# Kernel tuning notes

Hardware: AMD Instinct MI355X
Metric: run time of the kernel (lower is better)

The kernel has to match this reference:

```python
import jax, jax.numpy as jnp
import numpy as np

NUM_EXPERTS = 8
IN_FEATURES = 2048
OUT_FEATURES = 5632
GROUP_SIZE = 64
NUM_TOKENS = 4096


def setup_inputs() -> dict:
    key = jax.random.key(0)
    k1, k2, k3, k4 = jax.random.split(key, 4)
    inp = jax.random.normal(k1, (NUM_TOKENS, IN_FEATURES), dtype=jnp.float32)
    # tokens are pre-sorted contiguously per expert; balanced routing
    tokens_per_expert = jnp.full((NUM_EXPERTS,), NUM_TOKENS // NUM_EXPERTS, dtype=jnp.int32)
    # int4 quantized weights stored as integer codes in [0, 16)
    weights = jax.random.randint(k2, (NUM_EXPERTS, IN_FEATURES, OUT_FEATURES), 0, 16, dtype=jnp.int32)
    n_groups = IN_FEATURES // GROUP_SIZE
    scales = jax.random.uniform(k3, (NUM_EXPERTS, n_groups, OUT_FEATURES, 1), dtype=jnp.float32,
                                minval=0.005, maxval=0.02)
    zeros = jax.random.normal(k4, (NUM_EXPERTS, n_groups, OUT_FEATURES, 1), dtype=jnp.float32) * 0.01
    scales_and_zeros = jnp.concatenate([scales, zeros], axis=-1)  # [E, K//G, N, 2]
    return {"input": inp, "tokens_per_expert": tokens_per_expert,
            "weights": weights, "scales_and_zeros": scales_and_zeros}


def _dequant(weights, scales_and_zeros):
    # torchao int4 convention: w = (q - 8) * scale + zero, grouped along K
    E, K, N = weights.shape
    n_groups = scales_and_zeros.shape[1]
    g = K // n_groups
    q = weights.astype(jnp.float32).reshape(E, n_groups, g, N)
    s = scales_and_zeros[..., 0][:, :, None, :]  # [E, K//G, 1, N]
    z = scales_and_zeros[..., 1][:, :, None, :]
    return ((q - 8.0) * s + z).reshape(E, K, N)


def reference(input, tokens_per_expert, weights, scales_and_zeros):
    num_tokens, K = input.shape
    E = weights.shape[0]
    W = _dequant(weights, scales_and_zeros)  # [E, K, N] float32
    # expert id of each (contiguous-sorted) token from cumsum boundaries
    cum = jnp.cumsum(tokens_per_expert)                      # [E]
    seg = jnp.searchsorted(cum, jnp.arange(num_tokens), side='right')  # [T]
    start = jnp.concatenate([jnp.zeros((1,), cum.dtype), cum[:-1]])
    pos = jnp.arange(num_tokens) - start[seg]                # slot within expert block
    # capacity-based grouped GEMM (balanced routing in setup: C = T // E)
    C = num_tokens // E
    buf = jnp.zeros((E, C, K), input.dtype).at[seg, pos].set(input)
    y = jnp.einsum('eck,ekn->ecn', buf, W)                   # per-expert GEMM
    return y[seg, pos]                                       # [T, N]
```

## Files before the change

kernel.cpp:

```cpp
#include <hip/hip_runtime.h>

#define NE    8
#define KDIM  2048
#define NDIM  5632
#define NTOK  4096
#define CAP   512
#define NGRP  32
#define BM    128
#define BN    128
#define BK    32
#define MT    4
#define NT    44
#define LDSS  40

#define K8      (KDIM / 8)
#define NBLK_N  (NDIM / 256)
#define PACK_BLOCKS (NE * K8 * NBLK_N)
#define ACV_BLOCKS  (NTOK * KDIM / (8 * 256))
#define PACKED_BYTES ((size_t)NE * K8 * NDIM * 4)
#define ABF_BYTES    ((size_t)NTOK * KDIM * 2)

typedef __attribute__((ext_vector_type(8))) short bf16x8;
typedef __attribute__((ext_vector_type(4))) short bf16x4;
typedef __attribute__((ext_vector_type(4))) float f32x4;

static __device__ __forceinline__ short f2bf(float f) {
    union { float f; unsigned u; } x; x.f = f;
    unsigned r = (x.u + 0x7fffu + ((x.u >> 16) & 1u)) >> 16;
    return (short)r;
}

__global__ __launch_bounds__(256)
void pack_kernel(const int* __restrict__ wq, const float* __restrict__ inp,
                 unsigned* __restrict__ pw, unsigned short* __restrict__ abf)
{
    const int bid = blockIdx.x;
    if (bid < PACK_BLOCKS) {
        const int e  = bid / (K8 * NBLK_N);
        const int r  = bid % (K8 * NBLK_N);
        const int k8 = r / NBLK_N;
        const int nb = r % NBLK_N;
        const int n  = nb * 256 + threadIdx.x;
        const int* src = wq + ((size_t)e * KDIM + k8 * 8) * NDIM + n;
        unsigned v = 0;
        #pragma unroll
        for (int j = 0; j < 8; ++j)
            v |= (unsigned)(src[(size_t)j * NDIM] & 15) << (4 * j);
        pw[((size_t)e * K8 + k8) * NDIM + n] = v;
    } else {
        const size_t t = (size_t)(bid - PACK_BLOCKS) * 256 + threadIdx.x;
        const float4* p = (const float4*)inp + t * 2;
        const float4 v0 = p[0], v1 = p[1];
        bf16x8 h;
        h[0] = f2bf(v0.x); h[1] = f2bf(v0.y); h[2] = f2bf(v0.z); h[3] = f2bf(v0.w);
        h[4] = f2bf(v1.x); h[5] = f2bf(v1.y); h[6] = f2bf(v1.z); h[7] = f2bf(v1.w);
        *((bf16x8*)abf + t) = h;
    }
}

__global__ __launch_bounds__(256, 2)
void hqq_gemm2(const unsigned short* __restrict__ abf,
               const unsigned*       __restrict__ pw,
               const float*          __restrict__ sz,
               float*                __restrict__ out)
{
    const int bid = blockIdx.x;
    const int e   = bid / (MT * NT);
    const int rem = bid % (MT * NT);
    const int nt  = rem >> 2;
    const int mt  = rem & 3;

    __shared__ __align__(16) short Alds[BM * LDSS];
    __shared__ __align__(16) short Blds[BN * LDSS];

    const int tid = threadIdx.x;
    const int m0  = e * CAP + mt * BM;
    const int n0  = nt * BN;

    const int a_kq  = tid & 3;
    const int a_row = tid >> 2;
    const int b_n   = tid & 127;
    const int b_h   = tid >> 7;

    const unsigned short* Ab = abf + (size_t)m0 * KDIM;
    const unsigned*       Wb = pw  + (size_t)e * K8 * NDIM + n0 + b_n;
    const float*          SZb = sz + (size_t)e * NGRP * (NDIM * 2) + (size_t)(n0 + b_n) * 2;

    f32x4 acc[4][4];
    #pragma unroll
    for (int i = 0; i < 4; ++i)
        #pragma unroll
        for (int j = 0; j < 4; ++j)
            acc[i][j] = (f32x4){0.f, 0.f, 0.f, 0.f};

    const int wave = tid >> 6;
    const int lane = tid & 63;
    const int wm = (wave >> 1) << 6;
    const int wn = (wave & 1) << 6;
    const int lr = lane & 15;
    const int lq = lane >> 4;

    for (int k0 = 0; k0 < KDIM; k0 += BK) {
        const int g = k0 >> 6;

        #pragma unroll
        for (int p = 0; p < 2; ++p) {
            const int row = a_row + p * 64;
            const bf16x8 v = *(const bf16x8*)(Ab + (size_t)row * KDIM + k0 + a_kq * 8);
            *(bf16x8*)&Alds[row * LDSS + a_kq * 8] = v;
        }

        const float2 s2 = *(const float2*)(SZb + (size_t)g * (NDIM * 2));
        const float s  = s2.x;
        const float z8 = s2.y - 8.f * s2.x;
        const unsigned* wp = Wb + ((size_t)(k0 >> 3) + b_h * 2) * NDIM;
        const unsigned u0 = wp[0];
        const unsigned u1 = wp[NDIM];
        bf16x8 bb0, bb1;
        #pragma unroll
        for (int j = 0; j < 8; ++j) {
            bb0[j] = f2bf(fmaf((float)((u0 >> (4 * j)) & 15u), s, z8));
            bb1[j] = f2bf(fmaf((float)((u1 >> (4 * j)) & 15u), s, z8));
        }
        *(bf16x8*)&Blds[b_n * LDSS + b_h * 16]     = bb0;
        *(bf16x8*)&Blds[b_n * LDSS + b_h * 16 + 8] = bb1;

        __syncthreads();

        bf16x8 af[4], bfv[4];
        #pragma unroll
        for (int i = 0; i < 4; ++i)
            af[i] = *(const bf16x8*)&Alds[(wm + i * 16 + lr) * LDSS + lq * 8];
        #pragma unroll
        for (int j = 0; j < 4; ++j)
            bfv[j] = *(const bf16x8*)&Blds[(wn + j * 16 + lr) * LDSS + lq * 8];
        #pragma unroll
        for (int i = 0; i < 4; ++i)
            #pragma unroll
            for (int j = 0; j < 4; ++j)
                acc[i][j] = __builtin_amdgcn_mfma_f32_16x16x32_bf16(af[i], bfv[j], acc[i][j], 0, 0, 0);

        __syncthreads();
    }

    const int orow0 = m0 + wm + lq * 4;
    const int ocol0 = n0 + wn + lr;
    #pragma unroll
    for (int i = 0; i < 4; ++i)
        #pragma unroll
        for (int r = 0; r < 4; ++r) {
            float* op = out + (size_t)(orow0 + i * 16 + r) * NDIM + ocol0;
            #pragma unroll
            for (int j = 0; j < 4; ++j)
                op[j * 16] = acc[i][j][r];
        }
}

__global__ __launch_bounds__(256, 2)
void hqq_gemm_fallback(const float* __restrict__ inp,
                       const int*   __restrict__ wq,
                       const float* __restrict__ sz,
                       float*       __restrict__ out)
{
    const int bid = blockIdx.x;
    const int e   = bid / (MT * NT);
    const int rem = bid % (MT * NT);
    const int nt  = rem >> 2;
    const int mt  = rem & 3;

    __shared__ __align__(16) short Alds[BM * LDSS];
    __shared__ __align__(16) short Blds[BN * LDSS];

    const int tid = threadIdx.x;
    const int m0  = e * CAP + mt * BM;
    const int n0  = nt * BN;

    const int a_kq  = tid & 7;
    const int a_row = tid >> 3;
    const int b_n   = tid & 127;
    const int b_h   = tid >> 7;

    const float* Ab  = inp + (size_t)m0 * KDIM;
    const int*   Wb  = wq  + (size_t)e * KDIM * NDIM + n0 + b_n;
    const float* SZb = sz  + (size_t)e * NGRP * (NDIM * 2) + (size_t)(n0 + b_n) * 2;

    f32x4 acc[4][4];
    #pragma unroll
    for (int i = 0; i < 4; ++i)
        #pragma unroll
        for (int j = 0; j < 4; ++j)
            acc[i][j] = (f32x4){0.f, 0.f, 0.f, 0.f};

    const int wave = tid >> 6;
    const int lane = tid & 63;
    const int wm = (wave >> 1) << 6;
    const int wn = (wave & 1) << 6;
    const int lr = lane & 15;
    const int lq = lane >> 4;

    for (int k0 = 0; k0 < KDIM; k0 += BK) {
        const int g = k0 >> 6;
        #pragma unroll
        for (int p = 0; p < 4; ++p) {
            const int row = a_row + p * 32;
            const float4 v = *(const float4*)(Ab + (size_t)row * KDIM + k0 + a_kq * 4);
            bf16x4 h;
            h[0] = f2bf(v.x); h[1] = f2bf(v.y); h[2] = f2bf(v.z); h[3] = f2bf(v.w);
            *(bf16x4*)&Alds[row * LDSS + a_kq * 4] = h;
        }
        const float2 s2 = *(const float2*)(SZb + (size_t)g * (NDIM * 2));
        const float s  = s2.x;
        const float z8 = s2.y - 8.f * s2.x;
        #pragma unroll
        for (int oo = 0; oo < 2; ++oo) {
            const int ko = b_h * 8 + oo * 16;
            const int* wp = Wb + (size_t)(k0 + ko) * NDIM;
            bf16x8 bb;
            #pragma unroll
            for (int j = 0; j < 8; ++j) {
                const float q = (float)wp[(size_t)j * NDIM];
                bb[j] = f2bf(fmaf(q, s, z8));
            }
            *(bf16x8*)&Blds[b_n * LDSS + ko] = bb;
        }
        __syncthreads();
        bf16x8 af[4], bfv[4];
        #pragma unroll
        for (int i = 0; i < 4; ++i)
            af[i] = *(const bf16x8*)&Alds[(wm + i * 16 + lr) * LDSS + lq * 8];
        #pragma unroll
        for (int j = 0; j < 4; ++j)
            bfv[j] = *(const bf16x8*)&Blds[(wn + j * 16 + lr) * LDSS + lq * 8];
        #pragma unroll
        for (int i = 0; i < 4; ++i)
            #pragma unroll
            for (int j = 0; j < 4; ++j)
                acc[i][j] = __builtin_amdgcn_mfma_f32_16x16x32_bf16(af[i], bfv[j], acc[i][j], 0, 0, 0);
        __syncthreads();
    }

    const int orow0 = m0 + wm + lq * 4;
    const int ocol0 = n0 + wn + lr;
    #pragma unroll
    for (int i = 0; i < 4; ++i)
        #pragma unroll
        for (int r = 0; r < 4; ++r) {
            float* op = out + (size_t)(orow0 + i * 16 + r) * NDIM + ocol0;
            #pragma unroll
            for (int j = 0; j < 4; ++j)
                op[j * 16] = acc[i][j][r];
        }
}

extern "C" void kernel_launch(void* const* d_in, const int* in_sizes, int n_in,
                              void* d_out, int out_size, void* d_ws, size_t ws_size,
                              hipStream_t stream) {
    const float* inp = (const float*)d_in[0];
    const int*   wq  = (const int*)d_in[2];
    const float* sz  = (const float*)d_in[3];
    float*       out = (float*)d_out;

    if (ws_size >= PACKED_BYTES + ABF_BYTES) {
        unsigned*       pw  = (unsigned*)d_ws;
        unsigned short* abf = (unsigned short*)((char*)d_ws + PACKED_BYTES);
        pack_kernel<<<dim3(PACK_BLOCKS + ACV_BLOCKS), dim3(256), 0, stream>>>(wq, inp, pw, abf);
        hqq_gemm2<<<dim3(NE * MT * NT), dim3(256), 0, stream>>>(abf, pw, sz, out);
    } else {
        hqq_gemm_fallback<<<dim3(NE * MT * NT), dim3(256), 0, stream>>>(inp, wq, sz, out);
    }
}
```

Before: 673.1 us.

## Pre-dequantize weights to transposed bf16 and use direct-to-LDS GEMM loads

```diff
diff --git a/kernel.cpp b/kernel.cpp
--- a/kernel.cpp
+++ b/kernel.cpp
@@ -19,6 +19,11 @@
 #define ACV_BLOCKS  (NTOK * KDIM / (8 * 256))
 #define PACKED_BYTES ((size_t)NE * K8 * NDIM * 4)
 #define ABF_BYTES    ((size_t)NTOK * KDIM * 2)
+#define WBT_BYTES    ((size_t)NE * NDIM * KDIM * 2)
+
+#define KB_DQ (KDIM / 64)
+#define NB_DQ (NDIM / 256)
+#define DQT_BLOCKS (NE * KB_DQ * NB_DQ)
 
 typedef __attribute__((ext_vector_type(8))) short bf16x8;
 typedef __attribute__((ext_vector_type(4))) short bf16x4;
@@ -28,6 +33,127 @@
     union { float f; unsigned u; } x; x.f = f;
     unsigned r = (x.u + 0x7fffu + ((x.u >> 16) & 1u)) >> 16;
     return (short)r;
+}
+
+static __device__ __forceinline__ void gl2lds16(const unsigned short* g, short* l) {
+    __builtin_amdgcn_global_load_lds(
+        (const __attribute__((address_space(1))) unsigned int*)g,
+        (__attribute__((address_space(3))) unsigned int*)l, 16, 0, 0);
+}
+
+__global__ __launch_bounds__(256)
+void dq_kernel(const int* __restrict__ wq, const float* __restrict__ sz,
+               const float* __restrict__ inp,
+               unsigned short* __restrict__ wbt, unsigned short* __restrict__ abf)
+{
+    const int bid = blockIdx.x;
+    if (bid < DQT_BLOCKS) {
+        const int e  = bid / (KB_DQ * NB_DQ);
+        const int r  = bid % (KB_DQ * NB_DQ);
+        const int kb = r / NB_DQ;
+        const int nb = r % NB_DQ;
+        const int n  = nb * 256 + threadIdx.x;
+
+        const int* src = wq + ((size_t)e * KDIM + kb * 64) * NDIM + n;
+        const float2 s2 = *(const float2*)(sz + (((size_t)e * NGRP + kb) * NDIM + n) * 2);
+        const float s  = s2.x;
+        const float z8 = s2.y - 8.f * s2.x;
+        unsigned short* dst = wbt + ((size_t)e * NDIM + n) * KDIM + kb * 64;
+
+        #pragma unroll
+        for (int o = 0; o < 8; ++o) {
+            bf16x8 h;
+            #pragma unroll
+            for (int j = 0; j < 8; ++j) {
+                const float q = (float)src[(size_t)(o * 8 + j) * NDIM];
+                h[j] = f2bf(fmaf(q, s, z8));
+            }
+            *(bf16x8*)(dst + o * 8) = h;
+        }
+    } else {
+        const size_t t = (size_t)(bid - DQT_BLOCKS) * 256 + threadIdx.x;
+        const float4* p = (const float4*)inp + t * 2;
+        const float4 v0 = p[0], v1 = p[1];
+        bf16x8 h;
+        h[0] = f2bf(v0.x); h[1] = f2bf(v0.y); h[2] = f2bf(v0.z); h[3] = f2bf(v0.w);
+        h[4] = f2bf(v1.x); h[5] = f2bf(v1.y); h[6] = f2bf(v1.z); h[7] = f2bf(v1.w);
+        *((bf16x8*)abf + t) = h;
+    }
+}
+
+__global__ __launch_bounds__(256)
+void hqq_gemm3(const unsigned short* __restrict__ abf,
+               const unsigned short* __restrict__ wbt,
+               float* __restrict__ out)
+{
+    const int bid = blockIdx.x;
+    const int e   = bid & 7;
+    const int rem = bid >> 3;
+    const int nt  = rem >> 2;
+    const int mt  = rem & 3;
+
+    __shared__ __align__(16) short Alds[BM * BK];
+    __shared__ __align__(16) short Blds[BN * BK];
+
+    const int tid = threadIdx.x;
+    const int m0  = e * CAP + mt * BM;
+    const int n0  = nt * BN;
+
+    const unsigned short* Ab = abf + (size_t)m0 * KDIM;
+    const unsigned short* Bb = wbt + ((size_t)e * NDIM + n0) * KDIM;
+
+    f32x4 acc[4][4];
+    #pragma unroll
+    for (int i = 0; i < 4; ++i)
+        #pragma unroll
+        for (int j = 0; j < 4; ++j)
+            acc[i][j] = (f32x4){0.f, 0.f, 0.f, 0.f};
+
+    const int wave = tid >> 6;
+    const int lane = tid & 63;
+    const int wm = (wave >> 1) << 6;
+    const int wn = (wave & 1) << 6;
+    const int lr = lane & 15;
+    const int lq = lane >> 4;
+
+    for (int k0 = 0; k0 < KDIM; k0 += BK) {
+        #pragma unroll
+        for (int p = 0; p < 2; ++p) {
+            const int idx = p * 256 + tid;
+            const int row = idx >> 2;
+            const int kq  = idx & 3;
+            gl2lds16(Ab + (size_t)row * KDIM + k0 + kq * 8, &Alds[idx * 8]);
+            gl2lds16(Bb + (size_t)row * KDIM + k0 + kq * 8, &Blds[idx * 8]);
+        }
+        __syncthreads();
+
+        bf16x8 af[4], bv[4];
+        #pragma unroll
+        for (int i = 0; i < 4; ++i)
+            af[i] = *(const bf16x8*)&Alds[(wm + i * 16 + lr) * BK + lq * 8];
+        #pragma unroll
+        for (int j = 0; j < 4; ++j)
+            bv[j] = *(const bf16x8*)&Blds[(wn + j * 16 + lr) * BK + lq * 8];
+        #pragma unroll
+        for (int i = 0; i < 4; ++i)
+            #pragma unroll
+            for (int j = 0; j < 4; ++j)
+                acc[i][j] = __builtin_amdgcn_mfma_f32_16x16x32_bf16(af[i], bv[j], acc[i][j], 0, 0, 0);
+
+        __syncthreads();
+    }
+
+    const int orow0 = m0 + wm + lq * 4;
+    const int ocol0 = n0 + wn + lr;
+    #pragma unroll
+    for (int i = 0; i < 4; ++i)
+        #pragma unroll
+        for (int r = 0; r < 4; ++r) {
+            float* op = out + (size_t)(orow0 + i * 16 + r) * NDIM + ocol0;
+            #pragma unroll
+            for (int j = 0; j < 4; ++j)
+                op[j * 16] = acc[i][j][r];
+        }
 }
 
 __global__ __launch_bounds__(256)
@@ -102,14 +228,12 @@
 
     for (int k0 = 0; k0 < KDIM; k0 += BK) {
         const int g = k0 >> 6;
-
         #pragma unroll
         for (int p = 0; p < 2; ++p) {
             const int row = a_row + p * 64;
             const bf16x8 v = *(const bf16x8*)(Ab + (size_t)row * KDIM + k0 + a_kq * 8);
             *(bf16x8*)&Alds[row * LDSS + a_kq * 8] = v;
         }
-
         const float2 s2 = *(const float2*)(SZb + (size_t)g * (NDIM * 2));
         const float s  = s2.x;
         const float z8 = s2.y - 8.f * s2.x;
@@ -260,7 +384,12 @@
     const float* sz  = (const float*)d_in[3];
     float*       out = (float*)d_out;
 
-    if (ws_size >= PACKED_BYTES + ABF_BYTES) {
+    if (ws_size >= ABF_BYTES + WBT_BYTES) {
+        unsigned short* abf = (unsigned short*)d_ws;
+        unsigned short* wbt = (unsigned short*)((char*)d_ws + ABF_BYTES);
+        dq_kernel<<<dim3(DQT_BLOCKS + ACV_BLOCKS), dim3(256), 0, stream>>>(wq, sz, inp, wbt, abf);
+        hqq_gemm3<<<dim3(NE * MT * NT), dim3(256), 0, stream>>>(abf, wbt, out);
+    } else if (ws_size >= PACKED_BYTES + ABF_BYTES) {
         unsigned*       pw  = (unsigned*)d_ws;
         unsigned short* abf = (unsigned short*)((char*)d_ws + PACKED_BYTES);
         pack_kernel<<<dim3(PACK_BLOCKS + ACV_BLOCKS), dim3(256), 0, stream>>>(wq, inp, pw, abf);
```

Result: slower. 831.7 us (+23.6%).
